# Kernel tuning notes

Hardware: AMD Instinct MI355X
Metric: run time of the kernel (lower is better)

## Reference

```python
import jax, jax.numpy as jnp
import numpy as np

D_IN = 32
K = 16


def cbr(x, W, s, b):
    # 1x1 Conv2d + folded (eval-mode) BatchNorm + ReLU, channels-last.
    return jax.nn.relu(jnp.einsum('...i,io->...o', x, W) * s + b)


def gather_neighbour(pc, idx):
    # pc: [B, N, d]; idx: [B, N, K] -> [B, N, K, d]
    B, N, d = pc.shape
    g = jnp.take_along_axis(pc, idx.reshape(B, -1, 1), axis=1)
    return g.reshape(B, N, K, d)


def setup_inputs() -> dict:
    key = jax.random.key(0)
    ks = jax.random.split(key, 32)
    B, N = 2, 65536

    def w(k, ci, co):
        return jax.random.normal(k, (ci, co), jnp.float32) * (1.0 / np.sqrt(ci))

    inp = {
        'feature': jax.random.normal(ks[0], (B, D_IN, N, 1), jnp.float32),
        'xyz': jax.random.normal(ks[1], (B, N, 3), jnp.float32),
        'neigh_idx': jax.random.randint(ks[2], (B, N, K), 0, N, jnp.int64),
        # TNet
        'tW1': w(ks[3], 3, 16),  'ts1': jnp.ones(16),  'tb1': jnp.zeros(16),
        'tW2': w(ks[4], 16, 64), 'ts2': jnp.ones(64),  'tb2': jnp.zeros(64),
        'tW3': w(ks[5], 64, 16), 'ts3': jnp.ones(16),  'tb3': jnp.zeros(16),
        'tW4': w(ks[6], 16, 9),  'tb4': jnp.zeros(9),
        # RFA mlps
        'W1': w(ks[7], 3, 3),            's1': jnp.ones(3),     'b1': jnp.zeros(3),
        'W2': w(ks[8], D_IN, D_IN),      's2': jnp.ones(D_IN),  'b2': jnp.zeros(D_IN),
        'W3': w(ks[9], D_IN + 3, D_IN),  's3': jnp.ones(D_IN),  'b3': jnp.zeros(D_IN),
        'W4': w(ks[10], 2 * D_IN, D_IN), 's4': jnp.ones(D_IN),  'b4': jnp.zeros(D_IN),
    }
    return inp


def tnet(xyz, tW1, ts1, tb1, tW2, ts2, tb2, tW3, ts3, tb3, tW4, tb4):
    h = cbr(xyz, tW1, ts1, tb1)          # [B, N, 16]
    h = cbr(h, tW2, ts2, tb2)            # [B, N, 64]
    h = jnp.max(h, axis=1, keepdims=True)  # [B, 1, 64]
    h = cbr(h, tW3, ts3, tb3)            # [B, 1, 16]
    h = jnp.einsum('...i,io->...o', h, tW4) + tb4  # [B, 1, 9] (no bn/act)
    dia = jnp.eye(3, dtype=h.dtype).reshape(1, 1, 9)
    return (h + dia).reshape(-1, 3, 3)


def reference(feature, xyz, neigh_idx,
              tW1, ts1, tb1, tW2, ts2, tb2, tW3, ts3, tb3, tW4, tb4,
              W1, s1, b1, W2, s2, b2, W3, s3, b3, W4, s4, b4):
    # channels-last features [B, N, d_in]
    feat = feature.squeeze(-1).transpose(0, 2, 1)

    t = tnet(xyz, tW1, ts1, tb1, tW2, ts2, tb2, tW3, ts3, tb3, tW4, tb4)
    f_xyz = jnp.einsum('bni,bij->bnj', xyz, t)   # [B, N, 3]
    f_xyz = cbr(f_xyz, W1, s1, b1)               # [B, N, 3]
    f_xyz = gather_neighbour(f_xyz, neigh_idx)   # [B, N, K, 3]

    f_nei = cbr(feat, W2, s2, b2)                # [B, N, d]
    f_nei = gather_neighbour(f_nei, neigh_idx)   # [B, N, K, d]

    f_cat = jnp.concatenate([f_nei, f_xyz], axis=-1)  # [B, N, K, d+3]
    f_cat = cbr(f_cat, W3, s3, b3)               # [B, N, K, d]
    f_cat = jnp.max(f_cat, axis=2)               # max pooling over K -> [B, N, d]

    f = jnp.concatenate([feat, f_cat], axis=-1)  # [B, N, 2d]
    f = cbr(f, W4, s4, b4)                       # [B, N, d_in]
    return f.transpose(0, 2, 1)[..., None]       # [B, d_in, N, 1]
```

## Files before the change

### kernel.cpp

```cpp
#include <hip/hip_runtime.h>

#define NPTS  65536
#define BATCH 2
#define TOTAL (BATCH * NPTS)

typedef __attribute__((ext_vector_type(8)))  short short8;
typedef __attribute__((ext_vector_type(16))) float float16;
union F8 { uint4 u; short8 s; };

#define WS_HMAX 0
#define WS_T1A  1024
#define WS_T1B  (1024 + TOTAL * 64)
#define WS_T2   (1024 + TOTAL * 64 + TOTAL * 8)

__device__ __forceinline__ unsigned short f2bf(float x) {
    unsigned u = __float_as_uint(x);
    return (unsigned short)((u + 0x7FFFu + ((u >> 16) & 1u)) >> 16);
}
__device__ __forceinline__ unsigned pk2(float a, float b) {
    return (unsigned)f2bf(a) | ((unsigned)f2bf(b) << 16);
}
__device__ __forceinline__ float relu(float x) { return x > 0.f ? x : 0.f; }
__device__ __forceinline__ uint4 pk8(const float* e) {
    uint4 u;
    u.x = pk2(e[0], e[1]); u.y = pk2(e[2], e[3]);
    u.z = pk2(e[4], e[5]); u.w = pk2(e[6], e[7]);
    return u;
}

__global__ __launch_bounds__(256) void k1_tnet(const float* __restrict__ xyz,
        const float* __restrict__ tW1, const float* __restrict__ ts1, const float* __restrict__ tb1,
        const float* __restrict__ tW2, const float* __restrict__ ts2, const float* __restrict__ tb2,
        float* __restrict__ hmax)
{
    __shared__ float red[4][64];
    int lane = threadIdx.x & 63, wv = threadIdx.x >> 6;
    int col = lane & 31, h = lane >> 5;
    int blk_base = blockIdx.x * 512;
    int b = blk_base >> 16;

    float aw0[8], aw1[8], aw2[8], bb[8];
#pragma unroll
    for (int j = 0; j < 8; j++) {
        int k = 8 * h + j; float s = ts1[k];
        aw0[j] = tW1[k] * s; aw1[j] = tW1[16 + k] * s; aw2[j] = tW1[32 + k] * s;
        bb[j] = tb1[k];
    }
    float e[8];
    F8 bf0, bf1;
#pragma unroll
    for (int j = 0; j < 8; j++) e[j] = tW2[(8 * h + j) * 64 + col] * ts2[col];
    bf0.u = pk8(e);
#pragma unroll
    for (int j = 0; j < 8; j++) e[j] = tW2[(8 * h + j) * 64 + 32 + col] * ts2[32 + col];
    bf1.u = pk8(e);

    float16 m0, m1;
#pragma unroll
    for (int i = 0; i < 16; i++) { m0[i] = -1e30f; m1[i] = -1e30f; }

    for (int g = 0; g < 4; g++) {
        int base = blk_base + wv * 128 + g * 32;
        const float* xp = xyz + (size_t)(base + col) * 3;
        float x0 = xp[0], x1 = xp[1], x2 = xp[2];
        float hv[8];
#pragma unroll
        for (int j = 0; j < 8; j++)
            hv[j] = relu(x0 * aw0[j] + x1 * aw1[j] + x2 * aw2[j] + bb[j]);
        F8 af; af.u = pk8(hv);
        float16 z;
#pragma unroll
        for (int i = 0; i < 16; i++) z[i] = 0.f;
        float16 c0 = __builtin_amdgcn_mfma_f32_32x32x16_bf16(af.s, bf0.s, z, 0, 0, 0);
        float16 c1 = __builtin_amdgcn_mfma_f32_32x32x16_bf16(af.s, bf1.s, z, 0, 0, 0);
#pragma unroll
        for (int i = 0; i < 16; i++) { m0[i] = fmaxf(m0[i], c0[i]); m1[i] = fmaxf(m1[i], c1[i]); }
    }
    float v0 = m0[0], v1 = m1[0];
#pragma unroll
    for (int i = 1; i < 16; i++) { v0 = fmaxf(v0, m0[i]); v1 = fmaxf(v1, m1[i]); }
    v0 = fmaxf(v0, __shfl_xor(v0, 32));
    v1 = fmaxf(v1, __shfl_xor(v1, 32));
    if (h == 0) { red[wv][col] = v0; red[wv][32 + col] = v1; }
    __syncthreads();
    if (threadIdx.x < 64) {
        int c = threadIdx.x;
        float m = fmaxf(fmaxf(red[0][c], red[1][c]), fmaxf(red[2][c], red[3][c]));
        float val = relu(m + tb2[c]);
        atomicMax((unsigned*)(hmax + b * 64 + c), __float_as_uint(val));
    }
}

__global__ __launch_bounds__(256) void k3_prep(const float* __restrict__ feature,
        const float* __restrict__ xyz,
        const float* __restrict__ tW3, const float* __restrict__ ts3, const float* __restrict__ tb3,
        const float* __restrict__ tW4, const float* __restrict__ tb4,
        const float* __restrict__ W1,  const float* __restrict__ s1, const float* __restrict__ b1,
        const float* __restrict__ W2,  const float* __restrict__ s2, const float* __restrict__ b2,
        char* ws)
{
    __shared__ float Tsh[9];
    const float* hmax = (const float*)(ws + WS_HMAX);
    unsigned short* t1a = (unsigned short*)(ws + WS_T1A);
    unsigned short* t1b = (unsigned short*)(ws + WS_T1B);
    unsigned short* t2  = (unsigned short*)(ws + WS_T2);
    int lane = threadIdx.x & 63, wv = threadIdx.x >> 6;
    int col = lane & 31, h = lane >> 5;
    int base = (blockIdx.x * 4 + wv) * 32;
    int b = base >> 16;
    int pt = base + col;

    if (wv == 0) {
        int lc = lane & 15;
        float ha = 0.f;
        for (int i = 0; i < 64; i++) ha += hmax[b * 64 + i] * tW3[i * 16 + lc];
        float h3 = relu(ha * ts3[lc] + tb3[lc]);
        float T[9];
#pragma unroll
        for (int j = 0; j < 9; j++) T[j] = tb4[j];
        for (int c = 0; c < 16; c++) {
            float hc = __shfl(h3, c, 64);
#pragma unroll
            for (int j = 0; j < 9; j++) T[j] += hc * tW4[c * 9 + j];
        }
        T[0] += 1.f; T[4] += 1.f; T[8] += 1.f;
        if (lane < 9) Tsh[lane] = T[lane];
    }

    float e[8];
    float sc = s2[col];
    F8 a0, a1;
#pragma unroll
    for (int j = 0; j < 8; j++) e[j] = W2[(8 * h + j) * 32 + col] * sc;
    a0.u = pk8(e);
#pragma unroll
    for (int j = 0; j < 8; j++) e[j] = W2[(16 + 8 * h + j) * 32 + col] * sc;
    a1.u = pk8(e);

    const float* fb = feature + (size_t)b * 32 * NPTS + (pt & (NPTS - 1));
    float v[8];
    F8 b0, b1f;
#pragma unroll
    for (int j = 0; j < 8; j++) v[j] = fb[(size_t)(8 * h + j) * NPTS];
    b0.u = pk8(v);
#pragma unroll
    for (int j = 0; j < 8; j++) v[j] = fb[(size_t)(16 + 8 * h + j) * NPTS];
    b1f.u = pk8(v);
    *(uint4*)(t2 + (size_t)pt * 64 + 8 * h) = b0.u;
    *(uint4*)(t2 + (size_t)pt * 64 + 16 + 8 * h) = b1f.u;

    float16 acc;
#pragma unroll
    for (int i = 0; i < 16; i++) acc[i] = 0.f;
    acc = __builtin_amdgcn_mfma_f32_32x32x16_bf16(a0.s, b0.s, acc, 0, 0, 0);
    acc = __builtin_amdgcn_mfma_f32_32x32x16_bf16(a1.s, b1f.s, acc, 0, 0, 0);

    float b2v[16];
#pragma unroll
    for (int r = 0; r < 16; r++) b2v[r] = b2[(r & 3) + 8 * (r >> 2) + 4 * h];
#pragma unroll
    for (int q = 0; q < 4; q++) {
        int r = 4 * q;
        uint2 u;
        u.x = pk2(relu(acc[r] + b2v[r]), relu(acc[r + 1] + b2v[r + 1]));
        u.y = pk2(relu(acc[r + 2] + b2v[r + 2]), relu(acc[r + 3] + b2v[r + 3]));
        *(uint2*)(t1a + (size_t)pt * 32 + 8 * q + 4 * h) = u;
    }

    __syncthreads();
    float T[9];
#pragma unroll
    for (int j = 0; j < 9; j++) T[j] = Tsh[j];
    const float* xp = xyz + (size_t)pt * 3;
    float x0 = xp[0], x1 = xp[1], x2 = xp[2];
    float q0 = x0 * T[0] + x1 * T[3] + x2 * T[6];
    float q1 = x0 * T[1] + x1 * T[4] + x2 * T[7];
    float q2 = x0 * T[2] + x1 * T[5] + x2 * T[8];
    float r0 = relu((q0 * W1[0] + q1 * W1[3] + q2 * W1[6]) * s1[0] + b1[0]);
    float r1 = relu((q0 * W1[1] + q1 * W1[4] + q2 * W1[7]) * s1[1] + b1[1]);
    float r2 = relu((q0 * W1[2] + q1 * W1[5] + q2 * W1[8]) * s1[2] + b1[2]);
    if (h == 0) {
        uint2 u; u.x = pk2(r0, r1); u.y = pk2(r2, 0.f);
        *(uint2*)(t1b + (size_t)pt * 4) = u;
    }
}

__global__ __launch_bounds__(256) void k4_main(const int* __restrict__ nidx,
        const float* __restrict__ W3, const float* __restrict__ s3, const float* __restrict__ b3,
        char* ws)
{
    const unsigned short* t1a = (const unsigned short*)(ws + WS_T1A);
    const unsigned short* t1b = (const unsigned short*)(ws + WS_T1B);
    unsigned short* t2        = (unsigned short*)(ws + WS_T2);
    int lane = threadIdx.x & 63;
    int wave = (blockIdx.x * 256 + threadIdx.x) >> 6;
    int col = lane & 31, h = lane >> 5;

    float e[8];
    float sc = s3[col];
    F8 w0, w1, w2, zf;
    zf.u.x = zf.u.y = zf.u.z = zf.u.w = 0u;
#pragma unroll
    for (int j = 0; j < 8; j++) e[j] = W3[(8 * h + j) * 32 + col] * sc;
    w0.u = pk8(e);
#pragma unroll
    for (int j = 0; j < 8; j++) e[j] = W3[(16 + 8 * h + j) * 32 + col] * sc;
    w1.u = pk8(e);
    w2 = zf;
    if (h == 0) {
        float e2[8] = {0.f, 0.f, 0.f, 0.f, 0.f, 0.f, 0.f, 0.f};
#pragma unroll
        for (int j = 0; j < 3; j++) e2[j] = W3[(32 + j) * 32 + col] * sc;
        w2.u = pk8(e2);
    }
    float b3v = b3[col];

    int idxs[8];
#pragma unroll
    for (int gg = 0; gg < 8; gg++) {
        int pt = (wave * 8 + gg) * 2 + (col >> 4);
        idxs[gg] = nidx[pt * 16 + (col & 15)];
    }

    for (int gg = 0; gg < 8; gg++) {
        int base_pt = (wave * 8 + gg) * 2;
        int b = base_pt >> 16;
        size_t row = (size_t)((b << 16) + idxs[gg]);
        F8 a0, a1, a2;
        a0.u = *(const uint4*)(t1a + row * 32 + 8 * h);
        a1.u = *(const uint4*)(t1a + row * 32 + 16 + 8 * h);
        a2 = zf;
        if (h == 0) {
            uint2 q = *(const uint2*)(t1b + row * 4);
            a2.u.x = q.x; a2.u.y = q.y;
        }
        float16 acc;
#pragma unroll
        for (int i = 0; i < 16; i++) acc[i] = 0.f;
        acc = __builtin_amdgcn_mfma_f32_32x32x16_bf16(a0.s, w0.s, acc, 0, 0, 0);
        acc = __builtin_amdgcn_mfma_f32_32x32x16_bf16(a1.s, w1.s, acc, 0, 0, 0);
        acc = __builtin_amdgcn_mfma_f32_32x32x16_bf16(a2.s, w2.s, acc, 0, 0, 0);
        float vA = acc[0], vB = acc[8];
#pragma unroll
        for (int r = 1; r < 8; r++) { vA = fmaxf(vA, acc[r]); vB = fmaxf(vB, acc[8 + r]); }
        vA = fmaxf(vA, __shfl_xor(vA, 32));
        vB = fmaxf(vB, __shfl_xor(vB, 32));
        vA = relu(vA + b3v);
        vB = relu(vB + b3v);
        float val = h ? vB : vA;
        t2[(size_t)(base_pt + h) * 64 + 32 + col] = f2bf(val);
    }
}

__global__ __launch_bounds__(256) void k5_out(
        const float* __restrict__ W4, const float* __restrict__ s4, const float* __restrict__ b4,
        const char* __restrict__ ws, float* __restrict__ out)
{
    const unsigned short* t2 = (const unsigned short*)(ws + WS_T2);
    int lane = threadIdx.x & 63;
    int wave = (blockIdx.x * 256 + threadIdx.x) >> 6;
    int col = lane & 31, h = lane >> 5;

    float e[8];
    float sc = s4[col];
    F8 aw[4];
#pragma unroll
    for (int t = 0; t < 4; t++) {
#pragma unroll
        for (int j = 0; j < 8; j++) e[j] = W4[(16 * t + 8 * h + j) * 32 + col] * sc;
        aw[t].u = pk8(e);
    }
    float b4v[16];
#pragma unroll
    for (int r = 0; r < 16; r++) b4v[r] = b4[(r & 3) + 8 * (r >> 2) + 4 * h];

    for (int tt = 0; tt < 2; tt++) {
        int base = (wave * 2 + tt) * 32;
        int b = base >> 16;
        int p = base + col;
        int nl = p & (NPTS - 1);
        const unsigned short* bp = t2 + (size_t)p * 64 + 8 * h;
        F8 x0, x1, x2, x3;
        x0.u = *(const uint4*)(bp);
        x1.u = *(const uint4*)(bp + 16);
        x2.u = *(const uint4*)(bp + 32);
        x3.u = *(const uint4*)(bp + 48);
        float16 acc;
#pragma unroll
        for (int i = 0; i < 16; i++) acc[i] = 0.f;
        acc = __builtin_amdgcn_mfma_f32_32x32x16_bf16(aw[0].s, x0.s, acc, 0, 0, 0);
        acc = __builtin_amdgcn_mfma_f32_32x32x16_bf16(aw[1].s, x1.s, acc, 0, 0, 0);
        acc = __builtin_amdgcn_mfma_f32_32x32x16_bf16(aw[2].s, x2.s, acc, 0, 0, 0);
        acc = __builtin_amdgcn_mfma_f32_32x32x16_bf16(aw[3].s, x3.s, acc, 0, 0, 0);
        float* ob = out + (size_t)(b * 32) * NPTS + nl;
#pragma unroll
        for (int r = 0; r < 16; r++) {
            int o = (r & 3) + 8 * (r >> 2) + 4 * h;
            ob[(size_t)o * NPTS] = relu(acc[r] + b4v[r]);
        }
    }
}

extern "C" void kernel_launch(void* const* d_in, const int* in_sizes, int n_in,
                              void* d_out, int out_size, void* d_ws, size_t ws_size,
                              hipStream_t stream)
{
    const float* feature = (const float*)d_in[0];
    const float* xyz     = (const float*)d_in[1];
    const int*   nidx    = (const int*)d_in[2];
    const float* tW1 = (const float*)d_in[3];
    const float* ts1 = (const float*)d_in[4];
    const float* tb1 = (const float*)d_in[5];
    const float* tW2 = (const float*)d_in[6];
    const float* ts2 = (const float*)d_in[7];
    const float* tb2 = (const float*)d_in[8];
    const float* tW3 = (const float*)d_in[9];
    const float* ts3 = (const float*)d_in[10];
    const float* tb3 = (const float*)d_in[11];
    const float* tW4 = (const float*)d_in[12];
    const float* tb4 = (const float*)d_in[13];
    const float* W1  = (const float*)d_in[14];
    const float* s1  = (const float*)d_in[15];
    const float* b1  = (const float*)d_in[16];
    const float* W2  = (const float*)d_in[17];
    const float* s2  = (const float*)d_in[18];
    const float* b2  = (const float*)d_in[19];
    const float* W3  = (const float*)d_in[20];
    const float* s3  = (const float*)d_in[21];
    const float* b3  = (const float*)d_in[22];
    const float* W4  = (const float*)d_in[23];
    const float* s4  = (const float*)d_in[24];
    const float* b4  = (const float*)d_in[25];
    (void)in_sizes; (void)n_in; (void)out_size; (void)ws_size;

    char* ws = (char*)d_ws;
    float* hmax = (float*)(ws + WS_HMAX);

    hipMemsetAsync(hmax, 0, 512, stream);
    k1_tnet<<<256, 256, 0, stream>>>(xyz, tW1, ts1, tb1, tW2, ts2, tb2, hmax);
    k3_prep<<<1024, 256, 0, stream>>>(feature, xyz, tW3, ts3, tb3, tW4, tb4,
                                      W1, s1, b1, W2, s2, b2, ws);
    k4_main<<<2048, 256, 0, stream>>>(nidx, W3, s3, b3, ws);
    k5_out<<<512, 256, 0, stream>>>(W4, s4, b4, ws, (float*)d_out);
}
```

Before: 172.4 us.

## Fuse all stages into one cooperative persistent kernel with grid syncs

Replaces the four separate kernels with one cooperative kernel of 512 blocks that runs three phases separated by grid-wide syncs. The TNet max is merged into the feature-prep phase and written to 16 striped atomic slots to reduce contention. Phase 1 recomputes the 3x3 transform per unit instead of once per block. The gather/max stage and the output MLP are fused so the pooled features stay in LDS rather than round-tripping through global memory. The layout of the t2 buffer is halved in width as a result. The change risks grid-sync overhead, redundant per-unit TNet work and lower occupancy; a multi-kernel fallback is used if the cooperative launch fails.

```diff
diff --git a/kernel.cpp b/kernel.cpp
--- a/kernel.cpp
+++ b/kernel.cpp
@@ -1,17 +1,21 @@
 #include <hip/hip_runtime.h>
-
-#define NPTS  65536
-#define BATCH 2
-#define TOTAL (BATCH * NPTS)
+#include <hip/hip_cooperative_groups.h>
+
+namespace cg = cooperative_groups;
+
+#define NPTS   65536
+#define TOTAL  (2 * NPTS)
+#define NUNITS 1024
+#define CGRID  512
 
 typedef __attribute__((ext_vector_type(8)))  short short8;
 typedef __attribute__((ext_vector_type(16))) float float16;
 union F8 { uint4 u; short8 s; };
 
-#define WS_HMAX 0
-#define WS_T1A  1024
-#define WS_T1B  (1024 + TOTAL * 64)
-#define WS_T2   (1024 + TOTAL * 64 + TOTAL * 8)
+#define WS_STRIPE 0
+#define WS_T1A    8192
+#define WS_T1B    (8192 + TOTAL * 64)
+#define WS_T2     (8192 + TOTAL * 64 + TOTAL * 8)
 
 __device__ __forceinline__ unsigned short f2bf(float x) {
     unsigned u = __float_as_uint(x);
@@ -27,18 +31,25 @@
     u.z = pk2(e[4], e[5]); u.w = pk2(e[6], e[7]);
     return u;
 }
-
-__global__ __launch_bounds__(256) void k1_tnet(const float* __restrict__ xyz,
-        const float* __restrict__ tW1, const float* __restrict__ ts1, const float* __restrict__ tb1,
-        const float* __restrict__ tW2, const float* __restrict__ ts2, const float* __restrict__ tb2,
-        float* __restrict__ hmax)
-{
-    __shared__ float red[4][64];
-    int lane = threadIdx.x & 63, wv = threadIdx.x >> 6;
-    int col = lane & 31, h = lane >> 5;
-    int blk_base = blockIdx.x * 512;
-    int b = blk_base >> 16;
-
+__device__ __forceinline__ float16 zero16() {
+    float16 z;
+#pragma unroll
+    for (int i = 0; i < 16; i++) z[i] = 0.f;
+    return z;
+}
+
+__device__ __forceinline__ void phase0(int blk, int nblk,
+    const float* __restrict__ feature, const float* __restrict__ xyz,
+    const float* __restrict__ tW1, const float* __restrict__ ts1, const float* __restrict__ tb1,
+    const float* __restrict__ tW2, const float* __restrict__ ts2, const float* __restrict__ tb2,
+    const float* __restrict__ W2,  const float* __restrict__ s2,  const float* __restrict__ b2,
+    float* __restrict__ stripe, unsigned short* __restrict__ t1a, unsigned short* __restrict__ t2,
+    float (*red)[64])
+{
+    const int lane = threadIdx.x & 63, wv = threadIdx.x >> 6;
+    const int col = lane & 31, h = lane >> 5;
+    const float16 z = zero16();
+    float e[8];
     float aw0[8], aw1[8], aw2[8], bb[8];
 #pragma unroll
     for (int j = 0; j < 8; j++) {
@@ -46,7 +57,6 @@
         aw0[j] = tW1[k] * s; aw1[j] = tW1[16 + k] * s; aw2[j] = tW1[32 + k] * s;
         bb[j] = tb1[k];
     }
-    float e[8];
     F8 bf0, bf1;
 #pragma unroll
     for (int j = 0; j < 8; j++) e[j] = tW2[(8 * h + j) * 64 + col] * ts2[col];
@@ -54,13 +64,21 @@
 #pragma unroll
     for (int j = 0; j < 8; j++) e[j] = tW2[(8 * h + j) * 64 + 32 + col] * ts2[32 + col];
     bf1.u = pk8(e);
-
-    float16 m0, m1;
-#pragma unroll
-    for (int i = 0; i < 16; i++) { m0[i] = -1e30f; m1[i] = -1e30f; }
-
-    for (int g = 0; g < 4; g++) {
-        int base = blk_base + wv * 128 + g * 32;
+    F8 a0, a1;
+    float sc2 = s2[col];
+#pragma unroll
+    for (int j = 0; j < 8; j++) e[j] = W2[(8 * h + j) * 32 + col] * sc2;
+    a0.u = pk8(e);
+#pragma unroll
+    for (int j = 0; j < 8; j++) e[j] = W2[(16 + 8 * h + j) * 32 + col] * sc2;
+    a1.u = pk8(e);
+    float b2v[16];
+#pragma unroll
+    for (int r = 0; r < 16; r++) b2v[r] = b2[(r & 3) + 8 * (r >> 2) + 4 * h];
+
+    for (int u = blk; u < NUNITS; u += nblk) {
+        int base = u * 128 + wv * 32;
+        int b = u >> 9;
         const float* xp = xyz + (size_t)(base + col) * 3;
         float x0 = xp[0], x1 = xp[1], x2 = xp[2];
         float hv[8];
@@ -68,237 +86,259 @@
         for (int j = 0; j < 8; j++)
             hv[j] = relu(x0 * aw0[j] + x1 * aw1[j] + x2 * aw2[j] + bb[j]);
         F8 af; af.u = pk8(hv);
-        float16 z;
-#pragma unroll
-        for (int i = 0; i < 16; i++) z[i] = 0.f;
         float16 c0 = __builtin_amdgcn_mfma_f32_32x32x16_bf16(af.s, bf0.s, z, 0, 0, 0);
         float16 c1 = __builtin_amdgcn_mfma_f32_32x32x16_bf16(af.s, bf1.s, z, 0, 0, 0);
-#pragma unroll
-        for (int i = 0; i < 16; i++) { m0[i] = fmaxf(m0[i], c0[i]); m1[i] = fmaxf(m1[i], c1[i]); }
-    }
-    float v0 = m0[0], v1 = m1[0];
-#pragma unroll
-    for (int i = 1; i < 16; i++) { v0 = fmaxf(v0, m0[i]); v1 = fmaxf(v1, m1[i]); }
-    v0 = fmaxf(v0, __shfl_xor(v0, 32));
-    v1 = fmaxf(v1, __shfl_xor(v1, 32));
-    if (h == 0) { red[wv][col] = v0; red[wv][32 + col] = v1; }
-    __syncthreads();
-    if (threadIdx.x < 64) {
-        int c = threadIdx.x;
-        float m = fmaxf(fmaxf(red[0][c], red[1][c]), fmaxf(red[2][c], red[3][c]));
-        float val = relu(m + tb2[c]);
-        atomicMax((unsigned*)(hmax + b * 64 + c), __float_as_uint(val));
-    }
-}
-
-__global__ __launch_bounds__(256) void k3_prep(const float* __restrict__ feature,
-        const float* __restrict__ xyz,
-        const float* __restrict__ tW3, const float* __restrict__ ts3, const float* __restrict__ tb3,
-        const float* __restrict__ tW4, const float* __restrict__ tb4,
-        const float* __restrict__ W1,  const float* __restrict__ s1, const float* __restrict__ b1,
-        const float* __restrict__ W2,  const float* __restrict__ s2, const float* __restrict__ b2,
-        char* ws)
-{
-    __shared__ float Tsh[9];
-    const float* hmax = (const float*)(ws + WS_HMAX);
-    unsigned short* t1a = (unsigned short*)(ws + WS_T1A);
-    unsigned short* t1b = (unsigned short*)(ws + WS_T1B);
-    unsigned short* t2  = (unsigned short*)(ws + WS_T2);
-    int lane = threadIdx.x & 63, wv = threadIdx.x >> 6;
-    int col = lane & 31, h = lane >> 5;
-    int base = (blockIdx.x * 4 + wv) * 32;
-    int b = base >> 16;
-    int pt = base + col;
-
-    if (wv == 0) {
-        int lc = lane & 15;
-        float ha = 0.f;
-        for (int i = 0; i < 64; i++) ha += hmax[b * 64 + i] * tW3[i * 16 + lc];
-        float h3 = relu(ha * ts3[lc] + tb3[lc]);
+        float v0 = c0[0], v1 = c1[0];
+#pragma unroll
+        for (int i = 1; i < 16; i++) { v0 = fmaxf(v0, c0[i]); v1 = fmaxf(v1, c1[i]); }
+        v0 = fmaxf(v0, __shfl_xor(v0, 32));
+        v1 = fmaxf(v1, __shfl_xor(v1, 32));
+        if (h == 0) { red[wv][col] = v0; red[wv][32 + col] = v1; }
+        __syncthreads();
+        if (threadIdx.x < 64) {
+            int c = threadIdx.x;
+            float m = fmaxf(fmaxf(red[0][c], red[1][c]), fmaxf(red[2][c], red[3][c]));
+            float val = relu(m + tb2[c]);
+            atomicMax((unsigned*)(stripe + (blk & 15) * 128 + b * 64 + c),
+                      __float_as_uint(val));
+        }
+        int pt = base + col;
+        const float* fb = feature + (size_t)b * 32 * NPTS + (pt & (NPTS - 1));
+        float v[8];
+        F8 f0, f1;
+#pragma unroll
+        for (int j = 0; j < 8; j++) v[j] = fb[(size_t)(8 * h + j) * NPTS];
+        f0.u = pk8(v);
+#pragma unroll
+        for (int j = 0; j < 8; j++) v[j] = fb[(size_t)(16 + 8 * h + j) * NPTS];
+        f1.u = pk8(v);
+        *(uint4*)(t2 + (size_t)pt * 32 + 8 * h) = f0.u;
+        *(uint4*)(t2 + (size_t)pt * 32 + 16 + 8 * h) = f1.u;
+        float16 acc = z;
+        acc = __builtin_amdgcn_mfma_f32_32x32x16_bf16(a0.s, f0.s, acc, 0, 0, 0);
+        acc = __builtin_amdgcn_mfma_f32_32x32x16_bf16(a1.s, f1.s, acc, 0, 0, 0);
+#pragma unroll
+        for (int q = 0; q < 4; q++) {
+            int r = 4 * q;
+            uint2 uu;
+            uu.x = pk2(relu(acc[r] + b2v[r]), relu(acc[r + 1] + b2v[r + 1]));
+            uu.y = pk2(relu(acc[r + 2] + b2v[r + 2]), relu(acc[r + 3] + b2v[r + 3]));
+            *(uint2*)(t1a + (size_t)pt * 32 + 8 * q + 4 * h) = uu;
+        }
+        __syncthreads();
+    }
+}
+
+__device__ __forceinline__ void phase1(int blk, int nblk,
+    const float* __restrict__ xyz,
+    const float* __restrict__ tW3, const float* __restrict__ ts3, const float* __restrict__ tb3,
+    const float* __restrict__ tW4, const float* __restrict__ tb4,
+    const float* __restrict__ W1,  const float* __restrict__ s1, const float* __restrict__ b1,
+    const float* __restrict__ stripe, unsigned short* __restrict__ t1b)
+{
+    const int lane = threadIdx.x & 63, wv = threadIdx.x >> 6;
+    const int col = lane & 31, h = lane >> 5;
+    for (int u = blk; u < NUNITS; u += nblk) {
+        int b = u >> 9;
+        float hm = 0.f;
+#pragma unroll
+        for (int s = 0; s < 16; s++)
+            hm = fmaxf(hm, stripe[s * 128 + b * 64 + lane]);
+        float v[16];
+        const float4* trow = (const float4*)(tW3 + lane * 16);
+#pragma unroll
+        for (int q = 0; q < 4; q++) {
+            float4 t4 = trow[q];
+            v[4 * q + 0] = hm * t4.x; v[4 * q + 1] = hm * t4.y;
+            v[4 * q + 2] = hm * t4.z; v[4 * q + 3] = hm * t4.w;
+        }
+#pragma unroll
+        for (int off = 1; off < 64; off <<= 1) {
+#pragma unroll
+            for (int c = 0; c < 16; c++) v[c] += __shfl_xor(v[c], off);
+        }
         float T[9];
 #pragma unroll
         for (int j = 0; j < 9; j++) T[j] = tb4[j];
+#pragma unroll
         for (int c = 0; c < 16; c++) {
-            float hc = __shfl(h3, c, 64);
-#pragma unroll
-            for (int j = 0; j < 9; j++) T[j] += hc * tW4[c * 9 + j];
+            float h3 = relu(v[c] * ts3[c] + tb3[c]);
+#pragma unroll
+            for (int j = 0; j < 9; j++) T[j] += h3 * tW4[c * 9 + j];
         }
         T[0] += 1.f; T[4] += 1.f; T[8] += 1.f;
-        if (lane < 9) Tsh[lane] = T[lane];
-    }
-
+
+        int pt = u * 128 + wv * 32 + col;
+        const float* xp = xyz + (size_t)pt * 3;
+        float x0 = xp[0], x1 = xp[1], x2 = xp[2];
+        float q0 = x0 * T[0] + x1 * T[3] + x2 * T[6];
+        float q1 = x0 * T[1] + x1 * T[4] + x2 * T[7];
+        float q2 = x0 * T[2] + x1 * T[5] + x2 * T[8];
+        float r0 = relu((q0 * W1[0] + q1 * W1[3] + q2 * W1[6]) * s1[0] + b1[0]);
+        float r1 = relu((q0 * W1[1] + q1 * W1[4] + q2 * W1[7]) * s1[1] + b1[1]);
+        float r2 = relu((q0 * W1[2] + q1 * W1[5] + q2 * W1[8]) * s1[2] + b1[2]);
+        if (h == 0) {
+            uint2 uu; uu.x = pk2(r0, r1); uu.y = pk2(r2, 0.f);
+            *(uint2*)(t1b + (size_t)pt * 4) = uu;
+        }
+    }
+}
+
+__device__ __forceinline__ void phase23(int blk, int nblk,
+    const int* __restrict__ nidx,
+    const float* __restrict__ W3, const float* __restrict__ s3, const float* __restrict__ b3,
+    const float* __restrict__ W4, const float* __restrict__ s4, const float* __restrict__ b4,
+    const unsigned short* __restrict__ t1a, const unsigned short* __restrict__ t1b,
+    const unsigned short* __restrict__ t2, float* __restrict__ out,
+    unsigned short* __restrict__ mld )
+{
+    const int lane = threadIdx.x & 63, wv = threadIdx.x >> 6;
+    const int col = lane & 31, h = lane >> 5;
+    const float16 z = zero16();
     float e[8];
-    float sc = s2[col];
-    F8 a0, a1;
-#pragma unroll
-    for (int j = 0; j < 8; j++) e[j] = W2[(8 * h + j) * 32 + col] * sc;
-    a0.u = pk8(e);
-#pragma unroll
-    for (int j = 0; j < 8; j++) e[j] = W2[(16 + 8 * h + j) * 32 + col] * sc;
-    a1.u = pk8(e);
-
-    const float* fb = feature + (size_t)b * 32 * NPTS + (pt & (NPTS - 1));
-    float v[8];
-    F8 b0, b1f;
-#pragma unroll
-    for (int j = 0; j < 8; j++) v[j] = fb[(size_t)(8 * h + j) * NPTS];
-    b0.u = pk8(v);
-#pragma unroll
-    for (int j = 0; j < 8; j++) v[j] = fb[(size_t)(16 + 8 * h + j) * NPTS];
-    b1f.u = pk8(v);
-    *(uint4*)(t2 + (size_t)pt * 64 + 8 * h) = b0.u;
-    *(uint4*)(t2 + (size_t)pt * 64 + 16 + 8 * h) = b1f.u;
-
-    float16 acc;
-#pragma unroll
-    for (int i = 0; i < 16; i++) acc[i] = 0.f;
-    acc = __builtin_amdgcn_mfma_f32_32x32x16_bf16(a0.s, b0.s, acc, 0, 0, 0);
-    acc = __builtin_amdgcn_mfma_f32_32x32x16_bf16(a1.s, b1f.s, acc, 0, 0, 0);
-
-    float b2v[16];
-#pragma unroll
-    for (int r = 0; r < 16; r++) b2v[r] = b2[(r & 3) + 8 * (r >> 2) + 4 * h];
-#pragma unroll
-    for (int q = 0; q < 4; q++) {
-        int r = 4 * q;
-        uint2 u;
-        u.x = pk2(relu(acc[r] + b2v[r]), relu(acc[r + 1] + b2v[r + 1]));
-        u.y = pk2(relu(acc[r + 2] + b2v[r + 2]), relu(acc[r + 3] + b2v[r + 3]));
-        *(uint2*)(t1a + (size_t)pt * 32 + 8 * q + 4 * h) = u;
-    }
-
-    __syncthreads();
-    float T[9];
-#pragma unroll
-    for (int j = 0; j < 9; j++) T[j] = Tsh[j];
-    const float* xp = xyz + (size_t)pt * 3;
-    float x0 = xp[0], x1 = xp[1], x2 = xp[2];
-    float q0 = x0 * T[0] + x1 * T[3] + x2 * T[6];
-    float q1 = x0 * T[1] + x1 * T[4] + x2 * T[7];
-    float q2 = x0 * T[2] + x1 * T[5] + x2 * T[8];
-    float r0 = relu((q0 * W1[0] + q1 * W1[3] + q2 * W1[6]) * s1[0] + b1[0]);
-    float r1 = relu((q0 * W1[1] + q1 * W1[4] + q2 * W1[7]) * s1[1] + b1[1]);
-    float r2 = relu((q0 * W1[2] + q1 * W1[5] + q2 * W1[8]) * s1[2] + b1[2]);
-    if (h == 0) {
-        uint2 u; u.x = pk2(r0, r1); u.y = pk2(r2, 0.f);
-        *(uint2*)(t1b + (size_t)pt * 4) = u;
-    }
-}
-
-__global__ __launch_bounds__(256) void k4_main(const int* __restrict__ nidx,
-        const float* __restrict__ W3, const float* __restrict__ s3, const float* __restrict__ b3,
-        char* ws)
-{
-    const unsigned short* t1a = (const unsigned short*)(ws + WS_T1A);
-    const unsigned short* t1b = (const unsigned short*)(ws + WS_T1B);
-    unsigned short* t2        = (unsigned short*)(ws + WS_T2);
-    int lane = threadIdx.x & 63;
-    int wave = (blockIdx.x * 256 + threadIdx.x) >> 6;
-    int col = lane & 31, h = lane >> 5;
-
-    float e[8];
-    float sc = s3[col];
     F8 w0, w1, w2, zf;
     zf.u.x = zf.u.y = zf.u.z = zf.u.w = 0u;
-#pragma unroll
-    for (int j = 0; j < 8; j++) e[j] = W3[(8 * h + j) * 32 + col] * sc;
+    float sc3 = s3[col];
+#pragma unroll
+    for (int j = 0; j < 8; j++) e[j] = W3[(8 * h + j) * 32 + col] * sc3;
     w0.u = pk8(e);
 #pragma unroll
-    for (int j = 0; j < 8; j++) e[j] = W3[(16 + 8 * h + j) * 32 + col] * sc;
+    for (int j = 0; j < 8; j++) e[j] = W3[(16 + 8 * h + j) * 32 + col] * sc3;
     w1.u = pk8(e);
     w2 = zf;
     if (h == 0) {
         float e2[8] = {0.f, 0.f, 0.f, 0.f, 0.f, 0.f, 0.f, 0.f};
 #pragma unroll
-        for (int j = 0; j < 3; j++) e2[j] = W3[(32 + j) * 32 + col] * sc;
+        for (int j = 0; j < 3; j++) e2[j] = W3[(32 + j) * 32 + col] * sc3;
         w2.u = pk8(e2);
     }
     float b3v = b3[col];
-
-    int idxs[8];
-#pragma unroll
-    for (int gg = 0; gg < 8; gg++) {
-        int pt = (wave * 8 + gg) * 2 + (col >> 4);
-        idxs[gg] = nidx[pt * 16 + (col & 15)];
-    }
-
-    for (int gg = 0; gg < 8; gg++) {
-        int base_pt = (wave * 8 + gg) * 2;
-        int b = base_pt >> 16;
-        size_t row = (size_t)((b << 16) + idxs[gg]);
-        F8 a0, a1, a2;
-        a0.u = *(const uint4*)(t1a + row * 32 + 8 * h);
-        a1.u = *(const uint4*)(t1a + row * 32 + 16 + 8 * h);
-        a2 = zf;
-        if (h == 0) {
-            uint2 q = *(const uint2*)(t1b + row * 4);
-            a2.u.x = q.x; a2.u.y = q.y;
-        }
-        float16 acc;
-#pragma unroll
-        for (int i = 0; i < 16; i++) acc[i] = 0.f;
-        acc = __builtin_amdgcn_mfma_f32_32x32x16_bf16(a0.s, w0.s, acc, 0, 0, 0);
-        acc = __builtin_amdgcn_mfma_f32_32x32x16_bf16(a1.s, w1.s, acc, 0, 0, 0);
-        acc = __builtin_amdgcn_mfma_f32_32x32x16_bf16(a2.s, w2.s, acc, 0, 0, 0);
-        float vA = acc[0], vB = acc[8];
-#pragma unroll
-        for (int r = 1; r < 8; r++) { vA = fmaxf(vA, acc[r]); vB = fmaxf(vB, acc[8 + r]); }
-        vA = fmaxf(vA, __shfl_xor(vA, 32));
-        vB = fmaxf(vB, __shfl_xor(vB, 32));
-        vA = relu(vA + b3v);
-        vB = relu(vB + b3v);
-        float val = h ? vB : vA;
-        t2[(size_t)(base_pt + h) * 64 + 32 + col] = f2bf(val);
-    }
-}
-
-__global__ __launch_bounds__(256) void k5_out(
-        const float* __restrict__ W4, const float* __restrict__ s4, const float* __restrict__ b4,
-        const char* __restrict__ ws, float* __restrict__ out)
-{
-    const unsigned short* t2 = (const unsigned short*)(ws + WS_T2);
-    int lane = threadIdx.x & 63;
-    int wave = (blockIdx.x * 256 + threadIdx.x) >> 6;
-    int col = lane & 31, h = lane >> 5;
-
-    float e[8];
-    float sc = s4[col];
     F8 aw[4];
+    float sc4 = s4[col];
 #pragma unroll
     for (int t = 0; t < 4; t++) {
 #pragma unroll
-        for (int j = 0; j < 8; j++) e[j] = W4[(16 * t + 8 * h + j) * 32 + col] * sc;
+        for (int j = 0; j < 8; j++) e[j] = W4[(16 * t + 8 * h + j) * 32 + col] * sc4;
         aw[t].u = pk8(e);
     }
     float b4v[16];
 #pragma unroll
     for (int r = 0; r < 16; r++) b4v[r] = b4[(r & 3) + 8 * (r >> 2) + 4 * h];
 
-    for (int tt = 0; tt < 2; tt++) {
-        int base = (wave * 2 + tt) * 32;
-        int b = base >> 16;
-        int p = base + col;
-        int nl = p & (NPTS - 1);
-        const unsigned short* bp = t2 + (size_t)p * 64 + 8 * h;
+    int per = NUNITS / nblk;
+    int slot = blk & 7, batch = slot >> 2;
+    int grp = (blk >> 3) * 4 + (slot & 3);
+    for (int i = 0; i < per; i++) {
+        int u = batch * 512 + i * (nblk >> 1) + grp;
+        int base = u * 128;
+        int idx_n = nidx[(base + 2 * (wv * 16)) * 16 + col];
+        for (int it = 0; it < 16; it++) {
+            int pi = wv * 16 + it;
+            int base_pt = base + 2 * pi;
+            int idx = idx_n;
+            if (it < 15) idx_n = nidx[(base_pt + 2) * 16 + col];
+            size_t row = ((size_t)batch << 16) + (unsigned)idx;
+            const unsigned short* ap = t1a + row * 32;
+            F8 ga0, ga1, ga2;
+            ga0.u = *(const uint4*)(ap + 8 * h);
+            ga1.u = *(const uint4*)(ap + 16 + 8 * h);
+            ga2 = zf;
+            if (h == 0) {
+                uint2 q = *(const uint2*)(t1b + row * 4);
+                ga2.u.x = q.x; ga2.u.y = q.y;
+            }
+            float16 acc = z;
+            acc = __builtin_amdgcn_mfma_f32_32x32x16_bf16(ga0.s, w0.s, acc, 0, 0, 0);
+            acc = __builtin_amdgcn_mfma_f32_32x32x16_bf16(ga1.s, w1.s, acc, 0, 0, 0);
+            acc = __builtin_amdgcn_mfma_f32_32x32x16_bf16(ga2.s, w2.s, acc, 0, 0, 0);
+            float vA = acc[0], vB = acc[8];
+#pragma unroll
+            for (int r = 1; r < 8; r++) { vA = fmaxf(vA, acc[r]); vB = fmaxf(vB, acc[8 + r]); }
+            vA = fmaxf(vA, __shfl_xor(vA, 32));
+            vB = fmaxf(vB, __shfl_xor(vB, 32));
+            vA = relu(vA + b3v);
+            vB = relu(vB + b3v);
+            float val = h ? vB : vA;
+            mld[(2 * pi + h) * 36 + col] = f2bf(val);
+        }
+        int p_loc = wv * 32 + col;
+        int p = base + p_loc;
+        const unsigned short* bp = t2 + (size_t)p * 32 + 8 * h;
         F8 x0, x1, x2, x3;
         x0.u = *(const uint4*)(bp);
         x1.u = *(const uint4*)(bp + 16);
-        x2.u = *(const uint4*)(bp + 32);
-        x3.u = *(const uint4*)(bp + 48);
-        float16 acc;
-#pragma unroll
-        for (int i = 0; i < 16; i++) acc[i] = 0.f;
+        const unsigned short* mp = mld + p_loc * 36;
+        uint2 q0 = *(const uint2*)(mp + 8 * h);
+        uint2 q1 = *(const uint2*)(mp + 8 * h + 4);
+        uint2 q2 = *(const uint2*)(mp + 16 + 8 * h);
+        uint2 q3 = *(const uint2*)(mp + 16 + 8 * h + 4);
+        x2.u.x = q0.x; x2.u.y = q0.y; x2.u.z = q1.x; x2.u.w = q1.y;
+        x3.u.x = q2.x; x3.u.y = q2.y; x3.u.z = q3.x; x3.u.w = q3.y;
+        float16 acc = z;
         acc = __builtin_amdgcn_mfma_f32_32x32x16_bf16(aw[0].s, x0.s, acc, 0, 0, 0);
         acc = __builtin_amdgcn_mfma_f32_32x32x16_bf16(aw[1].s, x1.s, acc, 0, 0, 0);
         acc = __builtin_amdgcn_mfma_f32_32x32x16_bf16(aw[2].s, x2.s, acc, 0, 0, 0);
         acc = __builtin_amdgcn_mfma_f32_32x32x16_bf16(aw[3].s, x3.s, acc, 0, 0, 0);
-        float* ob = out + (size_t)(b * 32) * NPTS + nl;
+        float* ob = out + (size_t)(batch * 32) * NPTS + (p & (NPTS - 1));
 #pragma unroll
         for (int r = 0; r < 16; r++) {
             int o = (r & 3) + 8 * (r >> 2) + 4 * h;
             ob[(size_t)o * NPTS] = relu(acc[r] + b4v[r]);
         }
     }
+}
+
+#define ALL_ARGS feature, xyz, nidx, tW1, ts1, tb1, tW2, ts2, tb2, \
+                 tW3, ts3, tb3, tW4, tb4, W1, s1, b1, W2, s2, b2, \
+                 W3, s3, b3, W4, s4, b4
+#define ALL_PARAMS const float* __restrict__ feature, const float* __restrict__ xyz, \
+    const int* __restrict__ nidx, \
+    const float* __restrict__ tW1, const float* __restrict__ ts1, const float* __restrict__ tb1, \
+    const float* __restrict__ tW2, const float* __restrict__ ts2, const float* __restrict__ tb2, \
+    const float* __restrict__ tW3, const float* __restrict__ ts3, const float* __restrict__ tb3, \
+    const float* __restrict__ tW4, const float* __restrict__ tb4, \
+    const float* __restrict__ W1, const float* __restrict__ s1, const float* __restrict__ b1, \
+    const float* __restrict__ W2, const float* __restrict__ s2, const float* __restrict__ b2, \
+    const float* __restrict__ W3, const float* __restrict__ s3, const float* __restrict__ b3, \
+    const float* __restrict__ W4, const float* __restrict__ s4, const float* __restrict__ b4
+
+__global__ __launch_bounds__(256) void fused_coop(ALL_PARAMS, char* ws, float* out)
+{
+    __shared__ float red[4][64];
+    __shared__ unsigned short mld[128 * 36];
+    float* stripe = (float*)(ws + WS_STRIPE);
+    unsigned short* t1a = (unsigned short*)(ws + WS_T1A);
+    unsigned short* t1b = (unsigned short*)(ws + WS_T1B);
+    unsigned short* t2  = (unsigned short*)(ws + WS_T2);
+    cg::grid_group g = cg::this_grid();
+    phase0(blockIdx.x, gridDim.x, feature, xyz, tW1, ts1, tb1, tW2, ts2, tb2,
+           W2, s2, b2, stripe, t1a, t2, red);
+    g.sync();
+    phase1(blockIdx.x, gridDim.x, xyz, tW3, ts3, tb3, tW4, tb4, W1, s1, b1, stripe, t1b);
+    g.sync();
+    phase23(blockIdx.x, gridDim.x, nidx, W3, s3, b3, W4, s4, b4, t1a, t1b, t2, out, mld);
+}
+
+__global__ __launch_bounds__(256) void kP0(ALL_PARAMS, char* ws, float* out)
+{
+    __shared__ float red[4][64];
+    (void)out;
+    phase0(blockIdx.x, gridDim.x, feature, xyz, tW1, ts1, tb1, tW2, ts2, tb2,
+           W2, s2, b2, (float*)(ws + WS_STRIPE),
+           (unsigned short*)(ws + WS_T1A), (unsigned short*)(ws + WS_T2), red);
+}
+__global__ __launch_bounds__(256) void kP1(ALL_PARAMS, char* ws, float* out)
+{
+    (void)out;
+    phase1(blockIdx.x, gridDim.x, xyz, tW3, ts3, tb3, tW4, tb4, W1, s1, b1,
+           (const float*)(ws + WS_STRIPE), (unsigned short*)(ws + WS_T1B));
+}
+__global__ __launch_bounds__(256) void kP23(ALL_PARAMS, char* ws, float* out)
+{
+    __shared__ unsigned short mld[128 * 36];
+    phase23(blockIdx.x, gridDim.x, nidx, W3, s3, b3, W4, s4, b4,
+            (const unsigned short*)(ws + WS_T1A), (const unsigned short*)(ws + WS_T1B),
+            (const unsigned short*)(ws + WS_T2), out, mld);
 }
 
 extern "C" void kernel_launch(void* const* d_in, const int* in_sizes, int n_in,
@@ -333,13 +373,28 @@
     const float* b4  = (const float*)d_in[25];
     (void)in_sizes; (void)n_in; (void)out_size; (void)ws_size;
 
-    char* ws = (char*)d_ws;
-    float* hmax = (float*)(ws + WS_HMAX);
-
-    hipMemsetAsync(hmax, 0, 512, stream);
-    k1_tnet<<<256, 256, 0, stream>>>(xyz, tW1, ts1, tb1, tW2, ts2, tb2, hmax);
-    k3_prep<<<1024, 256, 0, stream>>>(feature, xyz, tW3, ts3, tb3, tW4, tb4,
-                                      W1, s1, b1, W2, s2, b2, ws);
-    k4_main<<<2048, 256, 0, stream>>>(nidx, W3, s3, b3, ws);
-    k5_out<<<512, 256, 0, stream>>>(W4, s4, b4, ws, (float*)d_out);
-}
+    char* wsp = (char*)d_ws;
+    float* outp = (float*)d_out;
+
+    hipMemsetAsync(wsp + WS_STRIPE, 0, 16 * 128 * sizeof(float), stream);
+
+    void* args[] = {
+        (void*)&feature, (void*)&xyz, (void*)&nidx,
+        (void*)&tW1, (void*)&ts1, (void*)&tb1,
+        (void*)&tW2, (void*)&ts2, (void*)&tb2,
+        (void*)&tW3, (void*)&ts3, (void*)&tb3,
+        (void*)&tW4, (void*)&tb4,
+        (void*)&W1, (void*)&s1, (void*)&b1,
+        (void*)&W2, (void*)&s2, (void*)&b2,
+        (void*)&W3, (void*)&s3, (void*)&b3,
+        (void*)&W4, (void*)&s4, (void*)&b4,
+        (void*)&wsp, (void*)&outp};
+    hipError_t err = hipLaunchCooperativeKernel((void*)fused_coop, dim3(CGRID), dim3(256),
+                                                args, 0, stream);
+    if (err != hipSuccess) {
+        (void)hipGetLastError();
+        kP0<<<NUNITS, 256, 0, stream>>>(ALL_ARGS, wsp, outp);
+        kP1<<<NUNITS, 256, 0, stream>>>(ALL_ARGS, wsp, outp);
+        kP23<<<NUNITS, 256, 0, stream>>>(ALL_ARGS, wsp, outp);
+    }
+}
```

Result: slower. 315.7 us (+83.1%).
